# Kernel tuning notes

Measured on AMD Instinct MI355X. Metric: run time of the kernel, lower is better.

The kernel has to match this reference:

```python
import jax, jax.numpy as jnp
import numpy as np

DIM = 2048
NUM_EXPERTS = 8
N_TOKENS = 8192
SPARSITY = 0.8  # sparsity_constraint parameter (used only to derive static k)
K = max(1, int(SPARSITY * NUM_EXPERTS))  # = 6


def setup_inputs() -> dict:
    key = jax.random.key(0)
    ks = jax.random.split(key, 5)
    scale = 1.0 / np.sqrt(DIM)
    x = jax.random.normal(ks[0], (N_TOKENS, DIM), dtype=jnp.float32)
    Wg = jax.random.uniform(ks[1], (NUM_EXPERTS, DIM), jnp.float32, -scale, scale)
    bg = jax.random.uniform(ks[2], (NUM_EXPERTS,), jnp.float32, -scale, scale)
    We = jax.random.uniform(ks[3], (NUM_EXPERTS, DIM, DIM), jnp.float32, -scale, scale)
    be = jax.random.uniform(ks[4], (NUM_EXPERTS, DIM), jnp.float32, -scale, scale)
    return {"x": x, "Wg": Wg, "bg": bg, "We": We, "be": be}


def reference(x, Wg, bg, We, be):
    # gate scores: [N, E]
    gate_scores = x @ Wg.T + bg
    # top-k expert indices per token: [N, K]
    _, topk_idx = jax.lax.top_k(gate_scores, K)
    # mask[n, e] = expert e is among token n's top-k: [N, E]
    mask = jnp.any(topk_idx[:, :, None] == jnp.arange(NUM_EXPERTS)[None, None, :], axis=1)
    # all expert outputs: [N, E, D]  (We is [E, out, in]; Linear = x @ W.T + b)
    expert_out = jnp.einsum('nd,efd->nef', x, We) + be[None, :, :]
    # combine: unweighted sum of selected experts' outputs (no gate weighting in source)
    out = jnp.sum(expert_out * mask[:, :, None].astype(x.dtype), axis=1)
    return out
```

## Files before the change

kernel.cpp:

```cpp
#include <hip/hip_runtime.h>
#include <hip/hip_bf16.h>
#include <stdint.h>

#define DIM 2048
#define NEXP 8
#define NTOK 8192
#define KSEL 6
#define NPAIR 28
#define SLOTS 92

typedef short bf16x8 __attribute__((ext_vector_type(8)));
typedef unsigned short u16x8 __attribute__((ext_vector_type(8)));
typedef float f32x4 __attribute__((ext_vector_type(4)));
typedef const __attribute__((address_space(1))) unsigned int GU32;
typedef __attribute__((address_space(3))) unsigned int LU32;

static constexpr int PA[NPAIR] = {0,0,0,0,0,0,0,1,1,1,1,1,1,2,2,2,2,2,3,3,3,3,4,4,4,5,5,6};
static constexpr int PB[NPAIR] = {1,2,3,4,5,6,7,2,3,4,5,6,7,3,4,5,6,7,4,5,6,7,5,6,7,6,7,7};

__device__ __forceinline__ unsigned short f2b(float f) {
  union { float f; uint32_t u; } v; v.f = f;
  return (unsigned short)((v.u + 0x7fffu + ((v.u >> 16) & 1u)) >> 16);
}

__global__ __launch_bounds__(256) void gate_kernel(
    const float* __restrict__ x, const float* __restrict__ Wg,
    const float* __restrict__ bg, unsigned short* __restrict__ xB,
    int* __restrict__ pid) {
  int t = threadIdx.x;
  int w = t >> 6, l = t & 63;
  int n = blockIdx.x * 4 + w;
  const float* xr = x + (size_t)n * DIM;
  float xv[32];
#pragma unroll
  for (int j = 0; j < 8; ++j) {
    float4 v = *(const float4*)(xr + 4 * l + 256 * j);
    xv[4 * j + 0] = v.x; xv[4 * j + 1] = v.y;
    xv[4 * j + 2] = v.z; xv[4 * j + 3] = v.w;
  }
  unsigned short* xbr = xB + (size_t)n * DIM;
#pragma unroll
  for (int j = 0; j < 8; ++j) {
    ushort4 o;
    o.x = f2b(xv[4 * j + 0]); o.y = f2b(xv[4 * j + 1]);
    o.z = f2b(xv[4 * j + 2]); o.w = f2b(xv[4 * j + 3]);
    *(ushort4*)(xbr + 4 * l + 256 * j) = o;
  }
  float sc[NEXP];
#pragma unroll
  for (int e = 0; e < NEXP; ++e) {
    const float* wr = Wg + e * DIM;
    float s = 0.f;
#pragma unroll
    for (int j = 0; j < 8; ++j) {
      float4 v = *(const float4*)(wr + 4 * l + 256 * j);
      s += xv[4 * j + 0] * v.x + xv[4 * j + 1] * v.y +
           xv[4 * j + 2] * v.z + xv[4 * j + 3] * v.w;
    }
#pragma unroll
    for (int off = 32; off > 0; off >>= 1) s += __shfl_xor(s, off, 64);
    sc[e] = s + bg[e];
  }
  if (l == 0) {
    int ex0 = -1, ex1 = -1;
#pragma unroll
    for (int e = 0; e < NEXP; ++e) {
      int rank = 0;
#pragma unroll
      for (int j = 0; j < NEXP; ++j)
        rank += (sc[j] > sc[e]) || (sc[j] == sc[e] && j < e);
      if (rank >= KSEL) { if (ex0 < 0) ex0 = e; else if (ex1 < 0) ex1 = e; }
    }
    pid[n] = ex0 * (15 - ex0) / 2 + (ex1 - ex0 - 1);
  }
}

__global__ __launch_bounds__(1024) void bucket_kernel(
    const int* __restrict__ pid, const float* __restrict__ be,
    int* __restrict__ cnt, int* __restrict__ meta,
    int* __restrict__ slotP, int* __restrict__ slotM0,
    int* __restrict__ list, float* __restrict__ biasPair) {
  int t = threadIdx.x;
  if (blockIdx.x == 1) {
#pragma unroll
    for (int it = 0; it < 2; ++it) {
      int f = t + 1024 * it;
      float v[NEXP]; float s = 0.f;
#pragma unroll
      for (int e = 0; e < NEXP; ++e) { v[e] = be[e * DIM + f]; s += v[e]; }
#pragma unroll
      for (int pp = 0; pp < NPAIR; ++pp)
        biasPair[pp * DIM + f] = s - v[PA[pp]] - v[PB[pp]];
    }
    return;
  }
  __shared__ int lcnt[NPAIR];
  __shared__ int lpos[NPAIR];
  if (t < NPAIR) { lcnt[t] = 0; lpos[t] = 0; }
  __syncthreads();
  int p[8];
#pragma unroll
  for (int j = 0; j < 8; ++j) {
    p[j] = pid[t + 1024 * j];
    atomicAdd(&lcnt[p[j]], 1);
  }
  __syncthreads();
  if (t == 0) {
    int ts = 0;
    for (int q = 0; q < NPAIR; ++q) {
      cnt[q] = lcnt[q];
      for (int s0 = 0; s0 < lcnt[q]; s0 += 128) {
        slotP[ts] = q; slotM0[ts] = s0; ++ts;
      }
    }
    meta[0] = ts;
  }
  __syncthreads();
#pragma unroll
  for (int j = 0; j < 8; ++j) {
    int pos = atomicAdd(&lpos[p[j]], 1);
    list[p[j] * NTOK + pos] = t + 1024 * j;
  }
}

__global__ __launch_bounds__(256) void pairw_kernel(
    const float* __restrict__ We, unsigned short* __restrict__ Wp,
    int fbase, int frows) {
  size_t pos = ((size_t)blockIdx.x * 256 + threadIdx.x) * 8;
  size_t src = (size_t)fbase * DIM + pos;
  float v[NEXP][8];
  float s[8];
#pragma unroll
  for (int i = 0; i < 8; ++i) s[i] = 0.f;
#pragma unroll
  for (int e = 0; e < NEXP; ++e) {
    float4 v0 = *(const float4*)(We + (size_t)e * DIM * DIM + src);
    float4 v1 = *(const float4*)(We + (size_t)e * DIM * DIM + src + 4);
    v[e][0] = v0.x; v[e][1] = v0.y; v[e][2] = v0.z; v[e][3] = v0.w;
    v[e][4] = v1.x; v[e][5] = v1.y; v[e][6] = v1.z; v[e][7] = v1.w;
#pragma unroll
    for (int i = 0; i < 8; ++i) s[i] += v[e][i];
  }
  size_t chunk = (size_t)frows * DIM;
#pragma unroll
  for (int pp = 0; pp < NPAIR; ++pp) {
    int a = PA[pp], b = PB[pp];
    u16x8 o;
#pragma unroll
    for (int i = 0; i < 8; ++i) o[i] = f2b(s[i] - v[a][i] - v[b][i]);
    *(u16x8*)(Wp + (size_t)pp * chunk + pos) = o;
  }
}

__global__ __launch_bounds__(256, 4) void gemm_pair(
    const unsigned short* __restrict__ A, const unsigned short* __restrict__ Wp,
    const int* __restrict__ cnt, const int* __restrict__ list,
    const int* __restrict__ meta, const int* __restrict__ slotP,
    const int* __restrict__ slotM0, const float* __restrict__ biasPair,
    float* __restrict__ out, int fbase, int frows) {
  __shared__ unsigned short sA[128 * 64];
  __shared__ unsigned short sB[128 * 64];
  __shared__ int sRows[128];
  int slot = blockIdx.y;
  if (slot >= meta[0]) return;
  int ft = blockIdx.x;
  int p = slotP[slot];
  int m0 = slotM0[slot];
  int c = cnt[p];

  int t = threadIdx.x;
  int w = t >> 6, l = t & 63;
  int wm = w & 1, wn = w >> 1;
  int quad = l >> 4, lr = l & 15;
  int cs = (l & 7) ^ ((l >> 3) & 7);

  if (t < 128) {
    int idx = m0 + t;
    if (idx >= c) idx = c - 1;
    sRows[t] = list[p * NTOK + idx];
  }
  __syncthreads();

  size_t rowOffA[4], rowOffB[4];
#pragma unroll
  for (int i = 0; i < 4; ++i)
    rowOffA[i] = (size_t)sRows[i * 32 + w * 8 + (l >> 3)] * DIM;
  const unsigned short* Bb =
      Wp + (size_t)p * frows * DIM + (size_t)ft * 128 * DIM;
#pragma unroll
  for (int i = 0; i < 4; ++i)
    rowOffB[i] = (size_t)(i * 32 + w * 8 + (l >> 3)) * DIM;

  f32x4 acc[4][4];
#pragma unroll
  for (int mi = 0; mi < 4; ++mi)
#pragma unroll
    for (int ni = 0; ni < 4; ++ni) {
      acc[mi][ni][0] = 0.f; acc[mi][ni][1] = 0.f;
      acc[mi][ni][2] = 0.f; acc[mi][ni][3] = 0.f;
    }

  for (int k0 = 0; k0 < DIM; k0 += 64) {
#pragma unroll
    for (int i = 0; i < 4; ++i) {
      __builtin_amdgcn_global_load_lds((GU32*)(A + rowOffA[i] + k0 + cs * 8),
          (LU32*)(sA + (i * 32 + w * 8) * 64), 16, 0, 0);
      __builtin_amdgcn_global_load_lds((GU32*)(Bb + rowOffB[i] + k0 + cs * 8),
          (LU32*)(sB + (i * 32 + w * 8) * 64), 16, 0, 0);
    }
    __syncthreads();
#pragma unroll
    for (int ks = 0; ks < 2; ++ks) {
      bf16x8 aF[4], bF[4];
#pragma unroll
      for (int mi = 0; mi < 4; ++mi)
        aF[mi] = *(const bf16x8*)(sA + (wm * 64 + mi * 16 + lr) * 64 +
                                  (((ks << 2) | quad) ^ (lr & 7)) * 8);
#pragma unroll
      for (int ni = 0; ni < 4; ++ni)
        bF[ni] = *(const bf16x8*)(sB + (wn * 64 + ni * 16 + lr) * 64 +
                                  (((ks << 2) | quad) ^ (lr & 7)) * 8);
#pragma unroll
      for (int mi = 0; mi < 4; ++mi)
#pragma unroll
        for (int ni = 0; ni < 4; ++ni)
          acc[mi][ni] = __builtin_amdgcn_mfma_f32_16x16x32_bf16(aF[mi], bF[ni], acc[mi][ni], 0, 0, 0);
    }
    __syncthreads();
  }

  int f0 = fbase + ft * 128;
  float bb[4];
#pragma unroll
  for (int ni = 0; ni < 4; ++ni)
    bb[ni] = biasPair[p * DIM + f0 + wn * 64 + ni * 16 + lr];
#pragma unroll
  for (int mi = 0; mi < 4; ++mi) {
#pragma unroll
    for (int i = 0; i < 4; ++i) {
      int lrow = wm * 64 + mi * 16 + quad * 4 + i;
      if (m0 + lrow < c) {
        float* orow = out + (size_t)sRows[lrow] * DIM + f0;
#pragma unroll
        for (int ni = 0; ni < 4; ++ni)
          orow[wn * 64 + ni * 16 + lr] = acc[mi][ni][i] + bb[ni];
      }
    }
  }
}

extern "C" void kernel_launch(void* const* d_in, const int* in_sizes, int n_in,
                              void* d_out, int out_size, void* d_ws, size_t ws_size,
                              hipStream_t stream) {
  const float* x  = (const float*)d_in[0];
  const float* Wg = (const float*)d_in[1];
  const float* bg = (const float*)d_in[2];
  const float* We = (const float*)d_in[3];
  const float* be = (const float*)d_in[4];
  float* out = (float*)d_out;

  char* ws = (char*)d_ws;
  unsigned short* xB = (unsigned short*)ws; ws += (size_t)NTOK * DIM * 2;
  int* pid = (int*)ws;          ws += (size_t)NTOK * 4;
  int* cnt = (int*)ws;          ws += 128;
  int* meta = (int*)ws;         ws += 128;
  int* slotP = (int*)ws;        ws += 512;
  int* slotM0 = (int*)ws;       ws += 512;
  int* list = (int*)ws;         ws += (size_t)NPAIR * NTOK * 4;
  float* biasPair = (float*)ws; ws += (size_t)NPAIR * DIM * 4;
  unsigned short* Wp = (unsigned short*)ws;

  size_t avail = ws_size - (size_t)(ws - (char*)d_ws);
  int NR = 2;
  while (NR < 16 && (size_t)NPAIR * DIM * (size_t)(DIM / NR) * 2 > avail) NR <<= 1;
  int frows = DIM / NR;

  gate_kernel<<<NTOK / 4, 256, 0, stream>>>(x, Wg, bg, xB, pid);
  bucket_kernel<<<2, 1024, 0, stream>>>(pid, be, cnt, meta, slotP, slotM0,
                                        list, biasPair);
  for (int r = 0; r < NR; ++r) {
    int fbase = r * frows;
    pairw_kernel<<<(frows * DIM) / 2048, 256, 0, stream>>>(We, Wp, fbase, frows);
    gemm_pair<<<dim3(frows / 128, SLOTS), 256, 0, stream>>>(
        xB, Wp, cnt, list, meta, slotP, slotM0, biasPair, out, fbase, frows);
  }
}
```

Baseline: 461.7 us.

## Fuse gate and first pair-weight build, reverse slot order, skip dead half-tiles

Merges the gate/bf16-cast kernel with the first pair-weight construction into one launch so both share the grid. It also lets the chunk count start at one, so the whole weight set can be built in a single pass when the workspace allows. The GEMM now walks slots in reverse so the partially filled tail slots are scheduled first. Waves whose 64-row half-tile has no valid tokens skip their MFMA work and their epilogue. These changes trim launch overhead and wasted MFMA work on partial tiles, in exchange for a larger workspace requirement and a branch inside the k-loop.

```diff
diff --git a/kernel.cpp b/kernel.cpp
--- a/kernel.cpp
+++ b/kernel.cpp
@@ -23,13 +23,42 @@
   return (unsigned short)((v.u + 0x7fffu + ((v.u >> 16) & 1u)) >> 16);
 }
 
-__global__ __launch_bounds__(256) void gate_kernel(
+__global__ __launch_bounds__(256) void gatepair_kernel(
     const float* __restrict__ x, const float* __restrict__ Wg,
-    const float* __restrict__ bg, unsigned short* __restrict__ xB,
-    int* __restrict__ pid) {
+    const float* __restrict__ bg, const float* __restrict__ We,
+    unsigned short* __restrict__ xB, int* __restrict__ pid,
+    unsigned short* __restrict__ Wp, int fbase, int frows, int pairwBlocks) {
+  int bid = blockIdx.x;
   int t = threadIdx.x;
+  if (bid < pairwBlocks) {
+    size_t pos = ((size_t)bid * 256 + t) * 8;
+    size_t src = (size_t)fbase * DIM + pos;
+    float v[NEXP][8];
+    float s[8];
+#pragma unroll
+    for (int i = 0; i < 8; ++i) s[i] = 0.f;
+#pragma unroll
+    for (int e = 0; e < NEXP; ++e) {
+      float4 v0 = *(const float4*)(We + (size_t)e * DIM * DIM + src);
+      float4 v1 = *(const float4*)(We + (size_t)e * DIM * DIM + src + 4);
+      v[e][0] = v0.x; v[e][1] = v0.y; v[e][2] = v0.z; v[e][3] = v0.w;
+      v[e][4] = v1.x; v[e][5] = v1.y; v[e][6] = v1.z; v[e][7] = v1.w;
+#pragma unroll
+      for (int i = 0; i < 8; ++i) s[i] += v[e][i];
+    }
+    size_t chunk = (size_t)frows * DIM;
+#pragma unroll
+    for (int pp = 0; pp < NPAIR; ++pp) {
+      int a = PA[pp], b = PB[pp];
+      u16x8 o;
+#pragma unroll
+      for (int i = 0; i < 8; ++i) o[i] = f2b(s[i] - v[a][i] - v[b][i]);
+      *(u16x8*)(Wp + (size_t)pp * chunk + pos) = o;
+    }
+    return;
+  }
   int w = t >> 6, l = t & 63;
-  int n = blockIdx.x * 4 + w;
+  int n = (bid - pairwBlocks) * 4 + w;
   const float* xr = x + (size_t)n * DIM;
   float xv[32];
 #pragma unroll
@@ -72,6 +101,35 @@
       if (rank >= KSEL) { if (ex0 < 0) ex0 = e; else if (ex1 < 0) ex1 = e; }
     }
     pid[n] = ex0 * (15 - ex0) / 2 + (ex1 - ex0 - 1);
+  }
+}
+
+__global__ __launch_bounds__(256) void pairw_kernel(
+    const float* __restrict__ We, unsigned short* __restrict__ Wp,
+    int fbase, int frows) {
+  size_t pos = ((size_t)blockIdx.x * 256 + threadIdx.x) * 8;
+  size_t src = (size_t)fbase * DIM + pos;
+  float v[NEXP][8];
+  float s[8];
+#pragma unroll
+  for (int i = 0; i < 8; ++i) s[i] = 0.f;
+#pragma unroll
+  for (int e = 0; e < NEXP; ++e) {
+    float4 v0 = *(const float4*)(We + (size_t)e * DIM * DIM + src);
+    float4 v1 = *(const float4*)(We + (size_t)e * DIM * DIM + src + 4);
+    v[e][0] = v0.x; v[e][1] = v0.y; v[e][2] = v0.z; v[e][3] = v0.w;
+    v[e][4] = v1.x; v[e][5] = v1.y; v[e][6] = v1.z; v[e][7] = v1.w;
+#pragma unroll
+    for (int i = 0; i < 8; ++i) s[i] += v[e][i];
+  }
+  size_t chunk = (size_t)frows * DIM;
+#pragma unroll
+  for (int pp = 0; pp < NPAIR; ++pp) {
+    int a = PA[pp], b = PB[pp];
+    u16x8 o;
+#pragma unroll
+    for (int i = 0; i < 8; ++i) o[i] = f2b(s[i] - v[a][i] - v[b][i]);
+    *(u16x8*)(Wp + (size_t)pp * chunk + pos) = o;
   }
 }
 
@@ -120,35 +178,6 @@
   for (int j = 0; j < 8; ++j) {
     int pos = atomicAdd(&lpos[p[j]], 1);
     list[p[j] * NTOK + pos] = t + 1024 * j;
-  }
-}
-
-__global__ __launch_bounds__(256) void pairw_kernel(
-    const float* __restrict__ We, unsigned short* __restrict__ Wp,
-    int fbase, int frows) {
-  size_t pos = ((size_t)blockIdx.x * 256 + threadIdx.x) * 8;
-  size_t src = (size_t)fbase * DIM + pos;
-  float v[NEXP][8];
-  float s[8];
-#pragma unroll
-  for (int i = 0; i < 8; ++i) s[i] = 0.f;
-#pragma unroll
-  for (int e = 0; e < NEXP; ++e) {
-    float4 v0 = *(const float4*)(We + (size_t)e * DIM * DIM + src);
-    float4 v1 = *(const float4*)(We + (size_t)e * DIM * DIM + src + 4);
-    v[e][0] = v0.x; v[e][1] = v0.y; v[e][2] = v0.z; v[e][3] = v0.w;
-    v[e][4] = v1.x; v[e][5] = v1.y; v[e][6] = v1.z; v[e][7] = v1.w;
-#pragma unroll
-    for (int i = 0; i < 8; ++i) s[i] += v[e][i];
-  }
-  size_t chunk = (size_t)frows * DIM;
-#pragma unroll
-  for (int pp = 0; pp < NPAIR; ++pp) {
-    int a = PA[pp], b = PB[pp];
-    u16x8 o;
-#pragma unroll
-    for (int i = 0; i < 8; ++i) o[i] = f2b(s[i] - v[a][i] - v[b][i]);
-    *(u16x8*)(Wp + (size_t)pp * chunk + pos) = o;
   }
 }
 
@@ -161,8 +190,9 @@
   __shared__ unsigned short sA[128 * 64];
   __shared__ unsigned short sB[128 * 64];
   __shared__ int sRows[128];
-  int slot = blockIdx.y;
-  if (slot >= meta[0]) return;
+  int total = meta[0];
+  if (blockIdx.y >= total) return;
+  int slot = total - 1 - blockIdx.y;
   int ft = blockIdx.x;
   int p = slotP[slot];
   int m0 = slotM0[slot];
@@ -173,6 +203,7 @@
   int wm = w & 1, wn = w >> 1;
   int quad = l >> 4, lr = l & 15;
   int cs = (l & 7) ^ ((l >> 3) & 7);
+  bool live = (wm == 0) || (m0 + 64 < c);
 
   if (t < 128) {
     int idx = m0 + t;
@@ -209,26 +240,29 @@
           (LU32*)(sB + (i * 32 + w * 8) * 64), 16, 0, 0);
     }
     __syncthreads();
-#pragma unroll
-    for (int ks = 0; ks < 2; ++ks) {
-      bf16x8 aF[4], bF[4];
-#pragma unroll
-      for (int mi = 0; mi < 4; ++mi)
-        aF[mi] = *(const bf16x8*)(sA + (wm * 64 + mi * 16 + lr) * 64 +
-                                  (((ks << 2) | quad) ^ (lr & 7)) * 8);
-#pragma unroll
-      for (int ni = 0; ni < 4; ++ni)
-        bF[ni] = *(const bf16x8*)(sB + (wn * 64 + ni * 16 + lr) * 64 +
-                                  (((ks << 2) | quad) ^ (lr & 7)) * 8);
-#pragma unroll
-      for (int mi = 0; mi < 4; ++mi)
+    if (live) {
+#pragma unroll
+      for (int ks = 0; ks < 2; ++ks) {
+        bf16x8 aF[4], bF[4];
+#pragma unroll
+        for (int mi = 0; mi < 4; ++mi)
+          aF[mi] = *(const bf16x8*)(sA + (wm * 64 + mi * 16 + lr) * 64 +
+                                    (((ks << 2) | quad) ^ (lr & 7)) * 8);
 #pragma unroll
         for (int ni = 0; ni < 4; ++ni)
-          acc[mi][ni] = __builtin_amdgcn_mfma_f32_16x16x32_bf16(aF[mi], bF[ni], acc[mi][ni], 0, 0, 0);
+          bF[ni] = *(const bf16x8*)(sB + (wn * 64 + ni * 16 + lr) * 64 +
+                                    (((ks << 2) | quad) ^ (lr & 7)) * 8);
+#pragma unroll
+        for (int mi = 0; mi < 4; ++mi)
+#pragma unroll
+          for (int ni = 0; ni < 4; ++ni)
+            acc[mi][ni] = __builtin_amdgcn_mfma_f32_16x16x32_bf16(aF[mi], bF[ni], acc[mi][ni], 0, 0, 0);
+      }
     }
     __syncthreads();
   }
 
+  if (!live) return;
   int f0 = fbase + ft * 128;
   float bb[4];
 #pragma unroll
@@ -271,14 +305,18 @@
   unsigned short* Wp = (unsigned short*)ws;
 
   size_t avail = ws_size - (size_t)(ws - (char*)d_ws);
-  int NR = 2;
+  int NR = 1;
   while (NR < 16 && (size_t)NPAIR * DIM * (size_t)(DIM / NR) * 2 > avail) NR <<= 1;
   int frows = DIM / NR;
 
-  gate_kernel<<<NTOK / 4, 256, 0, stream>>>(x, Wg, bg, xB, pid);
+  int pairwBlocks = (frows * DIM) / 2048;
+  gatepair_kernel<<<pairwBlocks + NTOK / 4, 256, 0, stream>>>(
+      x, Wg, bg, We, xB, pid, Wp, 0, frows, pairwBlocks);
   bucket_kernel<<<2, 1024, 0, stream>>>(pid, be, cnt, meta, slotP, slotM0,
                                         list, biasPair);
-  for (int r = 0; r < NR; ++r) {
+  gemm_pair<<<dim3(frows / 128, SLOTS), 256, 0, stream>>>(
+      xB, Wp, cnt, list, meta, slotP, slotM0, biasPair, out, 0, frows);
+  for (int r = 1; r < NR; ++r) {
     int fbase = r * frows;
     pairw_kernel<<<(frows * DIM) / 2048, 256, 0, stream>>>(We, Wp, fbase, frows);
     gemm_pair<<<dim3(frows / 128, SLOTS), 256, 0, stream>>>(
```

Result: no change. 459.3 us (-0.5%).
